# Kernel optimization log

Measured on AMD Instinct MI355X. Metric: run time of the kernel, lower is better.

The kernel has to match this reference:

```python
import jax, jax.numpy as jnp
import numpy as np

W_LOSS = 10.0
THRESHOLD = 1.0
ACOS_EPS = 1e-7


def _normalize(v, eps=1e-8):
    n = jnp.linalg.norm(v, axis=-1, keepdims=True)
    return v / jnp.maximum(n, eps)


def quat_to_rotmat(q):
    # q: (..., 4) in (w, x, y, z) order, as in Zhou et al. / EPN repo
    q = _normalize(q)
    w, x, y, z = q[..., 0], q[..., 1], q[..., 2], q[..., 3]
    R = jnp.stack([
        1 - 2 * (y * y + z * z), 2 * (x * y - z * w), 2 * (x * z + y * w),
        2 * (x * y + z * w), 1 - 2 * (x * x + z * z), 2 * (y * z - x * w),
        2 * (x * z - y * w), 2 * (y * z + x * w), 1 - 2 * (x * x + y * y),
    ], axis=-1)
    return R.reshape(q.shape[:-1] + (3, 3))


def acos_safe(x):
    return jnp.arccos(jnp.clip(x, -1.0 + ACOS_EPS, 1.0 - ACOS_EPS))


def angle_from_R(R):
    # R: (..., 3, 3) -> geodesic angle via trace
    tr = jnp.trace(R, axis1=-2, axis2=-1)
    return acos_safe(0.5 * (tr - 1.0))


def setup_inputs() -> dict:
    key = jax.random.key(0)
    k1, k2, k3, k4, k5 = jax.random.split(key, 5)
    B, NA, NR = 32768, 60, 4
    wts = jax.random.normal(k1, (B, NA), dtype=jnp.float32)
    label = jax.random.randint(k2, (B,), 0, NA, dtype=jnp.int64)
    y = jax.random.normal(k3, (B, NR, NA), dtype=jnp.float32)
    # gt_R and anchors are valid rotation matrices (via random quaternions)
    gt_R = quat_to_rotmat(jax.random.normal(k4, (B, NA, 4), dtype=jnp.float32))
    anchors = quat_to_rotmat(jax.random.normal(k5, (NA, 4), dtype=jnp.float32))
    return {"wts": wts, "label": label, "y": y, "gt_R": gt_R, "anchors": anchors}


def reference(wts, label, y, gt_R, anchors):
    b, na = wts.shape
    nr = y.shape[1]
    true_R = gt_R[:, 29]  # (b, 3, 3)

    # --- CrossEntropyLoss branch (classifier) ---
    logp = jax.nn.log_softmax(wts, axis=1)
    cls_loss = -jnp.mean(jnp.take_along_axis(logp, label[:, None], axis=1))
    preds = jnp.argmax(wts, axis=1)  # (b,)
    r_acc = jnp.mean((preds == label).astype(jnp.float32))

    # --- anchor-wise predicted rotations ---
    # y (b, nr, na) -> (b, na, nr) -> (b, na, 3, 3)
    pred_RAnchor = quat_to_rotmat(jnp.swapaxes(y, 1, 2))

    gt_bias = angle_from_R(gt_R)  # (b, na)
    mask = (gt_bias < THRESHOLD).astype(gt_R.dtype)[:, :, None, None]
    l2_loss = jnp.sum(jnp.square(gt_R * mask - pred_RAnchor * mask))
    loss = cls_loss + W_LOSS * l2_loss

    # --- final predicted rotation: gather best anchor, compose with anchor rot ---
    sel = jnp.take_along_axis(pred_RAnchor, preds[:, None, None, None], axis=1)[:, 0]  # (b,3,3)
    pred_R = jnp.einsum('bij,bjk->bik', anchors[preds], sel)

    # --- mean angular error ---
    ang_err = angle_from_R(jnp.einsum('bij,bkj->bik', pred_R, true_R))  # (b,)

    return (loss, cls_loss, W_LOSS * l2_loss, r_acc, ang_err)
```

## Files before the change

kernel.cpp:

```cpp
#include <hip/hip_runtime.h>
#include <math.h>

constexpr int Bc  = 32768;
constexpr int NAc = 60;

constexpr int BPB  = 4;
constexpr int NBLK = Bc / BPB;
constexpr int ROWF = NAc * 9;
constexpr int STG4 = BPB * ROWF / 4;

#define COS_ONE 0.5403023058681398f

__global__ __launch_bounds__(256) void mtl_all(
    const float* __restrict__ wts,
    const int*   __restrict__ label,
    const float* __restrict__ y,
    const float* __restrict__ gt_R,
    const float* __restrict__ anchors,
    float*       __restrict__ out,
    float*       __restrict__ l2p,
    float*       __restrict__ lpp,
    float*       __restrict__ crp)
{
    __shared__ __align__(16) float sg[BPB * ROWF + 16];
    const int tid  = threadIdx.x;
    const int lane = tid & 63;
    const int wave = tid >> 6;
    const int b0   = blockIdx.x * BPB;
    const int b    = b0 + wave;

    const float4* gb4 = (const float4*)(gt_R + (size_t)b0 * ROWF);
    float4* sg4 = (float4*)sg;
    sg4[tid]       = gb4[tid];
    sg4[tid + 256] = gb4[tid + 256];
    if (tid < STG4 - 512) sg4[tid + 512] = gb4[tid + 512];

    const int a = lane;
    int lab = label[b];
    float w = -INFINITY;
    float qw = 0, qx = 0, qy = 0, qz = 0;
    float A0=0,A1=0,A2=0,A3=0,A4=0,A5=0,A6=0,A7=0,A8=0;
    if (a < NAc) {
        w = wts[(size_t)b * NAc + a];
        const float* yb = y + (size_t)b * (4 * NAc) + a;
        qw = yb[0 * NAc];
        qx = yb[1 * NAc];
        qy = yb[2 * NAc];
        qz = yb[3 * NAc];
        const float* Ar = anchors + a * 9;
        A0 = Ar[0]; A1 = Ar[1]; A2 = Ar[2];
        A3 = Ar[3]; A4 = Ar[4]; A5 = Ar[5];
        A6 = Ar[6]; A7 = Ar[7]; A8 = Ar[8];
    }

    float n   = sqrtf(qw*qw + qx*qx + qy*qy + qz*qz);
    float inv = 1.0f / fmaxf(n, 1e-8f);
    float pw = qw*inv, px = qx*inv, py = qy*inv, pz = qz*inv;
    float R00 = 1.0f - 2.0f*(py*py + pz*pz);
    float R01 = 2.0f*(px*py - pz*pw);
    float R02 = 2.0f*(px*pz + py*pw);
    float R10 = 2.0f*(px*py + pz*pw);
    float R11 = 1.0f - 2.0f*(px*px + pz*pz);
    float R12 = 2.0f*(py*pz - px*pw);
    float R20 = 2.0f*(px*pz - py*pw);
    float R21 = 2.0f*(py*pz + px*pw);
    float R22 = 1.0f - 2.0f*(px*px + py*py);

    __syncthreads();

    float acc = 0.0f;
    if (a < NAc) {
        const float* g = sg + wave * ROWF + a * 9;
        float g0 = g[0], g1 = g[1], g2 = g[2];
        float g3 = g[3], g4 = g[4], g5 = g[5];
        float g6 = g[6], g7 = g[7], g8 = g[8];
        float xb = 0.5f * (g0 + g4 + g8 - 1.0f);
        if (xb > COS_ONE) {
            float d0 = g0-R00, d1 = g1-R01, d2 = g2-R02;
            float d3 = g3-R10, d4 = g4-R11, d5 = g5-R12;
            float d6 = g6-R20, d7 = g7-R21, d8 = g8-R22;
            acc = d0*d0 + d1*d1 + d2*d2
                + d3*d3 + d4*d4 + d5*d5
                + d6*d6 + d7*d7 + d8*d8;
        }
    }

    float mv = w;
    int   mi = lane;
    for (int off = 32; off; off >>= 1) {
        float ov = __shfl_xor(mv, off, 64);
        int   oi = __shfl_xor(mi, off, 64);
        if (ov > mv || (ov == mv && oi < mi)) { mv = ov; mi = oi; }
    }
    float e  = (a < NAc) ? expf(w - mv) : 0.0f;
    float se = e;
    for (int off = 32; off; off >>= 1) se += __shfl_xor(se, off, 64);
    float lse  = mv + logf(se);
    float wlab = __shfl(w, lab, 64);

    if (lane == mi) {
        float P00 = A0*R00 + A1*R10 + A2*R20;
        float P01 = A0*R01 + A1*R11 + A2*R21;
        float P02 = A0*R02 + A1*R12 + A2*R22;
        float P10 = A3*R00 + A4*R10 + A5*R20;
        float P11 = A3*R01 + A4*R11 + A5*R21;
        float P12 = A3*R02 + A4*R12 + A5*R22;
        float P20 = A6*R00 + A7*R10 + A8*R20;
        float P21 = A6*R01 + A7*R11 + A8*R21;
        float P22 = A6*R02 + A7*R12 + A8*R22;
        const float* tR = sg + wave * ROWF + 29 * 9;
        float tr = P00*tR[0] + P01*tR[1] + P02*tR[2]
                 + P10*tR[3] + P11*tR[4] + P12*tR[5]
                 + P20*tR[6] + P21*tR[7] + P22*tR[8];
        float cx = 0.5f * (tr - 1.0f);
        cx = fminf(fmaxf(cx, -1.0f + 1e-7f), 1.0f - 1e-7f);
        out[4 + b] = acosf(cx);
    }

    for (int off = 32; off; off >>= 1) acc += __shfl_xor(acc, off, 64);

    float* s_l2 = sg + BPB * ROWF;
    float* s_lp = s_l2 + 4;
    float* s_cr = s_lp + 4;
    if (lane == 0) {
        s_l2[wave] = acc;
        s_lp[wave] = wlab - lse;
        s_cr[wave] = (mi == lab) ? 1.0f : 0.0f;
    }
    __syncthreads();
    if (tid == 0) {
        l2p[blockIdx.x] = s_l2[0] + s_l2[1] + s_l2[2] + s_l2[3];
        lpp[blockIdx.x] = s_lp[0] + s_lp[1] + s_lp[2] + s_lp[3];
        crp[blockIdx.x] = s_cr[0] + s_cr[1] + s_cr[2] + s_cr[3];
    }
}

__global__ __launch_bounds__(256) void mtl_final(
    const float* __restrict__ l2p,
    const float* __restrict__ lpp,
    const float* __restrict__ crp,
    float*       __restrict__ out)
{
    const int tid  = threadIdx.x;
    const int lane = tid & 63;
    const int wave = tid >> 6;

    double l2 = 0.0, lp = 0.0, cr = 0.0;
    const float4* l2p4 = (const float4*)l2p;
    const float4* lpp4 = (const float4*)lpp;
    const float4* crp4 = (const float4*)crp;
    for (int i = tid; i < NBLK / 4; i += 256) {
        float4 v = l2p4[i];
        l2 += (double)v.x + (double)v.y + (double)v.z + (double)v.w;
        float4 u = lpp4[i];
        lp += (double)u.x + (double)u.y + (double)u.z + (double)u.w;
        float4 c = crp4[i];
        cr += (double)c.x + (double)c.y + (double)c.z + (double)c.w;
    }

    for (int off = 32; off; off >>= 1) {
        l2 += __shfl_xor(l2, off, 64);
        lp += __shfl_xor(lp, off, 64);
        cr += __shfl_xor(cr, off, 64);
    }
    __shared__ double s_l2[4], s_lp[4], s_cr[4];
    if (lane == 0) { s_l2[wave] = l2; s_lp[wave] = lp; s_cr[wave] = cr; }
    __syncthreads();
    if (tid == 0) {
        double t2 = s_l2[0] + s_l2[1] + s_l2[2] + s_l2[3];
        double tp = s_lp[0] + s_lp[1] + s_lp[2] + s_lp[3];
        double tc = s_cr[0] + s_cr[1] + s_cr[2] + s_cr[3];
        float cls = (float)(-tp / (double)Bc);
        float l2s = (float)(10.0 * t2);
        out[0] = cls + l2s;
        out[1] = cls;
        out[2] = l2s;
        out[3] = (float)(tc / (double)Bc);
    }
}

extern "C" void kernel_launch(void* const* d_in, const int* in_sizes, int n_in,
                              void* d_out, int out_size, void* d_ws, size_t ws_size,
                              hipStream_t stream) {
    const float* wts     = (const float*)d_in[0];
    const int*   label   = (const int*)d_in[1];
    const float* y       = (const float*)d_in[2];
    const float* gt_R    = (const float*)d_in[3];
    const float* anchors = (const float*)d_in[4];
    float* out = (float*)d_out;

    float* l2p = (float*)d_ws;
    float* lpp = l2p + NBLK;
    float* crp = lpp + NBLK;

    mtl_all  <<<NBLK, 256, 0, stream>>>(wts, label, y, gt_R, anchors,
                                        out, l2p, lpp, crp);
    mtl_final<<<1, 256, 0, stream>>>(l2p, lpp, crp, out);
}
```

Before: 140.1 us.

## Persistent grid with double-buffered async global-to-LDS staging of gt_R

The launch shrinks from one block per 4 batch rows to 2048 persistent blocks, each looping over 4 groups. The next group's gt_R tile is staged into a second LDS buffer with global_load_lds, and its wts, y and label are prefetched into registers while the current group is computed. The goal is to hide memory latency and overlap loads with compute, and also to cut the anchor loads and the partial-sum count. In exchange, occupancy and wave-level parallelism drop, and the code now depends on correct synchronisation around the async LDS loads.

```diff
diff --git a/kernel.cpp b/kernel.cpp
--- a/kernel.cpp
+++ b/kernel.cpp
@@ -1,15 +1,31 @@
 #include <hip/hip_runtime.h>
 #include <math.h>
 
-constexpr int Bc  = 32768;
-constexpr int NAc = 60;
+constexpr int Bc   = 32768;
+constexpr int NAc  = 60;
 
 constexpr int BPB  = 4;
-constexpr int NBLK = Bc / BPB;
+constexpr int PBLK = 2048;
+constexpr int ITER = Bc / (BPB * PBLK);
 constexpr int ROWF = NAc * 9;
-constexpr int STG4 = BPB * ROWF / 4;
+constexpr int GRPF = BPB * ROWF;
 
 #define COS_ONE 0.5403023058681398f
+
+typedef const __attribute__((address_space(1))) void* as1cv;
+typedef __attribute__((address_space(3)))       void* as3v;
+
+__device__ __forceinline__ void stage_group_async(const float* __restrict__ gt_R,
+                                                  int grp, float* lds,
+                                                  int wave, int lane)
+{
+    const float* gbase = gt_R + (size_t)grp * GRPF;
+    const int woff = wave * 512;
+    __builtin_amdgcn_global_load_lds((as1cv)(gbase + woff + lane * 4),
+                                     (as3v)(lds + woff), 16, 0, 0);
+    __builtin_amdgcn_global_load_lds((as1cv)(gbase + woff + 256 + lane * 4),
+                                     (as3v)(lds + woff + 256), 16, 0, 0);
+}
 
 __global__ __launch_bounds__(256) void mtl_all(
     const float* __restrict__ wts,
@@ -22,116 +38,144 @@
     float*       __restrict__ lpp,
     float*       __restrict__ crp)
 {
-    __shared__ __align__(16) float sg[BPB * ROWF + 16];
+    __shared__ __align__(16) float sg[2][GRPF];
+    __shared__ float s_red[12];
     const int tid  = threadIdx.x;
     const int lane = tid & 63;
     const int wave = tid >> 6;
-    const int b0   = blockIdx.x * BPB;
-    const int b    = b0 + wave;
-
-    const float4* gb4 = (const float4*)(gt_R + (size_t)b0 * ROWF);
-    float4* sg4 = (float4*)sg;
-    sg4[tid]       = gb4[tid];
-    sg4[tid + 256] = gb4[tid + 256];
-    if (tid < STG4 - 512) sg4[tid + 512] = gb4[tid + 512];
-
-    const int a = lane;
+    const int a    = lane;
+
+    float A0=0,A1=0,A2=0,A3=0,A4=0,A5=0,A6=0,A7=0,A8=0;
+    if (a < NAc) {
+        const float* Ar = anchors + a * 9;
+        A0=Ar[0]; A1=Ar[1]; A2=Ar[2];
+        A3=Ar[3]; A4=Ar[4]; A5=Ar[5];
+        A6=Ar[6]; A7=Ar[7]; A8=Ar[8];
+    }
+
+    int g = blockIdx.x;
+    {
+        stage_group_async(gt_R, g, sg[0], wave, lane);
+        const float4* gb4 = (const float4*)(gt_R + (size_t)g * GRPF);
+        if (tid < 28) ((float4*)sg[0])[512 + tid] = gb4[512 + tid];
+    }
+    int b   = g * BPB + wave;
     int lab = label[b];
-    float w = -INFINITY;
-    float qw = 0, qx = 0, qy = 0, qz = 0;
-    float A0=0,A1=0,A2=0,A3=0,A4=0,A5=0,A6=0,A7=0,A8=0;
+    float w = -INFINITY, qw=0, qx=0, qy=0, qz=0;
     if (a < NAc) {
         w = wts[(size_t)b * NAc + a];
         const float* yb = y + (size_t)b * (4 * NAc) + a;
-        qw = yb[0 * NAc];
-        qx = yb[1 * NAc];
-        qy = yb[2 * NAc];
-        qz = yb[3 * NAc];
-        const float* Ar = anchors + a * 9;
-        A0 = Ar[0]; A1 = Ar[1]; A2 = Ar[2];
-        A3 = Ar[3]; A4 = Ar[4]; A5 = Ar[5];
-        A6 = Ar[6]; A7 = Ar[7]; A8 = Ar[8];
-    }
-
-    float n   = sqrtf(qw*qw + qx*qx + qy*qy + qz*qz);
-    float inv = 1.0f / fmaxf(n, 1e-8f);
-    float pw = qw*inv, px = qx*inv, py = qy*inv, pz = qz*inv;
-    float R00 = 1.0f - 2.0f*(py*py + pz*pz);
-    float R01 = 2.0f*(px*py - pz*pw);
-    float R02 = 2.0f*(px*pz + py*pw);
-    float R10 = 2.0f*(px*py + pz*pw);
-    float R11 = 1.0f - 2.0f*(px*px + pz*pz);
-    float R12 = 2.0f*(py*pz - px*pw);
-    float R20 = 2.0f*(px*pz - py*pw);
-    float R21 = 2.0f*(py*pz + px*pw);
-    float R22 = 1.0f - 2.0f*(px*px + py*py);
-
+        qw = yb[0];  qx = yb[NAc];  qy = yb[2 * NAc];  qz = yb[3 * NAc];
+    }
     __syncthreads();
 
-    float acc = 0.0f;
-    if (a < NAc) {
-        const float* g = sg + wave * ROWF + a * 9;
-        float g0 = g[0], g1 = g[1], g2 = g[2];
-        float g3 = g[3], g4 = g[4], g5 = g[5];
-        float g6 = g[6], g7 = g[7], g8 = g[8];
-        float xb = 0.5f * (g0 + g4 + g8 - 1.0f);
-        if (xb > COS_ONE) {
-            float d0 = g0-R00, d1 = g1-R01, d2 = g2-R02;
-            float d3 = g3-R10, d4 = g4-R11, d5 = g5-R12;
-            float d6 = g6-R20, d7 = g7-R21, d8 = g8-R22;
-            acc = d0*d0 + d1*d1 + d2*d2
-                + d3*d3 + d4*d4 + d5*d5
-                + d6*d6 + d7*d7 + d8*d8;
-        }
-    }
-
-    float mv = w;
-    int   mi = lane;
-    for (int off = 32; off; off >>= 1) {
-        float ov = __shfl_xor(mv, off, 64);
-        int   oi = __shfl_xor(mi, off, 64);
-        if (ov > mv || (ov == mv && oi < mi)) { mv = ov; mi = oi; }
-    }
-    float e  = (a < NAc) ? expf(w - mv) : 0.0f;
-    float se = e;
-    for (int off = 32; off; off >>= 1) se += __shfl_xor(se, off, 64);
-    float lse  = mv + logf(se);
-    float wlab = __shfl(w, lab, 64);
-
-    if (lane == mi) {
-        float P00 = A0*R00 + A1*R10 + A2*R20;
-        float P01 = A0*R01 + A1*R11 + A2*R21;
-        float P02 = A0*R02 + A1*R12 + A2*R22;
-        float P10 = A3*R00 + A4*R10 + A5*R20;
-        float P11 = A3*R01 + A4*R11 + A5*R21;
-        float P12 = A3*R02 + A4*R12 + A5*R22;
-        float P20 = A6*R00 + A7*R10 + A8*R20;
-        float P21 = A6*R01 + A7*R11 + A8*R21;
-        float P22 = A6*R02 + A7*R12 + A8*R22;
-        const float* tR = sg + wave * ROWF + 29 * 9;
-        float tr = P00*tR[0] + P01*tR[1] + P02*tR[2]
-                 + P10*tR[3] + P11*tR[4] + P12*tR[5]
-                 + P20*tR[6] + P21*tR[7] + P22*tR[8];
-        float cx = 0.5f * (tr - 1.0f);
-        cx = fminf(fmaxf(cx, -1.0f + 1e-7f), 1.0f - 1e-7f);
-        out[4 + b] = acosf(cx);
-    }
-
-    for (int off = 32; off; off >>= 1) acc += __shfl_xor(acc, off, 64);
-
-    float* s_l2 = sg + BPB * ROWF;
-    float* s_lp = s_l2 + 4;
-    float* s_cr = s_lp + 4;
+    float l2acc = 0.0f, lpacc = 0.0f, cracc = 0.0f;
+
+    #pragma unroll
+    for (int it = 0; it < ITER; ++it) {
+        const int cur = it & 1, nxt = cur ^ 1;
+        const int gn  = g + PBLK;
+
+        float4 p2 = make_float4(0.f, 0.f, 0.f, 0.f);
+        int   labn = 0;
+        float wn = -INFINITY, qwn=0, qxn=0, qyn=0, qzn=0;
+        if (it + 1 < ITER) {
+            stage_group_async(gt_R, gn, sg[nxt], wave, lane);
+            const float4* nb4 = (const float4*)(gt_R + (size_t)gn * GRPF);
+            if (tid < 28) p2 = nb4[512 + tid];
+            const int bn = gn * BPB + wave;
+            labn = label[bn];
+            if (a < NAc) {
+                wn = wts[(size_t)bn * NAc + a];
+                const float* yb = y + (size_t)bn * (4 * NAc) + a;
+                qwn = yb[0];  qxn = yb[NAc];  qyn = yb[2 * NAc];  qzn = yb[3 * NAc];
+            }
+        }
+
+        float nq  = sqrtf(qw*qw + qx*qx + qy*qy + qz*qz);
+        float inv = 1.0f / fmaxf(nq, 1e-8f);
+        float pw = qw*inv, px = qx*inv, py = qy*inv, pz = qz*inv;
+        float R00 = 1.0f - 2.0f*(py*py + pz*pz);
+        float R01 = 2.0f*(px*py - pz*pw);
+        float R02 = 2.0f*(px*pz + py*pw);
+        float R10 = 2.0f*(px*py + pz*pw);
+        float R11 = 1.0f - 2.0f*(px*px + pz*pz);
+        float R12 = 2.0f*(py*pz - px*pw);
+        float R20 = 2.0f*(px*pz - py*pw);
+        float R21 = 2.0f*(py*pz + px*pw);
+        float R22 = 1.0f - 2.0f*(px*px + py*py);
+
+        if (a < NAc) {
+            const float* grow = sg[cur] + wave * ROWF + a * 9;
+            float g0 = grow[0], g1 = grow[1], g2 = grow[2];
+            float g3 = grow[3], g4 = grow[4], g5 = grow[5];
+            float g6 = grow[6], g7 = grow[7], g8 = grow[8];
+            float xb = 0.5f * (g0 + g4 + g8 - 1.0f);
+            if (xb > COS_ONE) {
+                float d0 = g0-R00, d1 = g1-R01, d2 = g2-R02;
+                float d3 = g3-R10, d4 = g4-R11, d5 = g5-R12;
+                float d6 = g6-R20, d7 = g7-R21, d8 = g8-R22;
+                l2acc += d0*d0 + d1*d1 + d2*d2
+                       + d3*d3 + d4*d4 + d5*d5
+                       + d6*d6 + d7*d7 + d8*d8;
+            }
+        }
+
+        float mv = w;
+        int   mi = lane;
+        for (int off = 32; off; off >>= 1) {
+            float ov = __shfl_xor(mv, off, 64);
+            int   oi = __shfl_xor(mi, off, 64);
+            if (ov > mv || (ov == mv && oi < mi)) { mv = ov; mi = oi; }
+        }
+        float e  = (a < NAc) ? expf(w - mv) : 0.0f;
+        float se = e;
+        for (int off = 32; off; off >>= 1) se += __shfl_xor(se, off, 64);
+        float lse  = mv + logf(se);
+        float wlab = __shfl(w, lab, 64);
+
+        lpacc += wlab - lse;
+        cracc += (mi == lab) ? 1.0f : 0.0f;
+
+        if (lane == mi) {
+            float P00 = A0*R00 + A1*R10 + A2*R20;
+            float P01 = A0*R01 + A1*R11 + A2*R21;
+            float P02 = A0*R02 + A1*R12 + A2*R22;
+            float P10 = A3*R00 + A4*R10 + A5*R20;
+            float P11 = A3*R01 + A4*R11 + A5*R21;
+            float P12 = A3*R02 + A4*R12 + A5*R22;
+            float P20 = A6*R00 + A7*R10 + A8*R20;
+            float P21 = A6*R01 + A7*R11 + A8*R21;
+            float P22 = A6*R02 + A7*R12 + A8*R22;
+            const float* tR = sg[cur] + wave * ROWF + 29 * 9;
+            float tr = P00*tR[0] + P01*tR[1] + P02*tR[2]
+                     + P10*tR[3] + P11*tR[4] + P12*tR[5]
+                     + P20*tR[6] + P21*tR[7] + P22*tR[8];
+            float cx = 0.5f * (tr - 1.0f);
+            cx = fminf(fmaxf(cx, -1.0f + 1e-7f), 1.0f - 1e-7f);
+            out[4 + b] = acosf(cx);
+        }
+
+        if (it + 1 < ITER) {
+            if (tid < 28) ((float4*)sg[nxt])[512 + tid] = p2;
+        }
+        __syncthreads();
+
+        w = wn; qw = qwn; qx = qxn; qy = qyn; qz = qzn;
+        lab = labn; g = gn; b = gn * BPB + wave;
+    }
+
+    for (int off = 32; off; off >>= 1) l2acc += __shfl_xor(l2acc, off, 64);
     if (lane == 0) {
-        s_l2[wave] = acc;
-        s_lp[wave] = wlab - lse;
-        s_cr[wave] = (mi == lab) ? 1.0f : 0.0f;
+        s_red[wave]     = l2acc;
+        s_red[4 + wave] = lpacc;
+        s_red[8 + wave] = cracc;
     }
     __syncthreads();
     if (tid == 0) {
-        l2p[blockIdx.x] = s_l2[0] + s_l2[1] + s_l2[2] + s_l2[3];
-        lpp[blockIdx.x] = s_lp[0] + s_lp[1] + s_lp[2] + s_lp[3];
-        crp[blockIdx.x] = s_cr[0] + s_cr[1] + s_cr[2] + s_cr[3];
+        l2p[blockIdx.x] = s_red[0] + s_red[1] + s_red[2]  + s_red[3];
+        lpp[blockIdx.x] = s_red[4] + s_red[5] + s_red[6]  + s_red[7];
+        crp[blockIdx.x] = s_red[8] + s_red[9] + s_red[10] + s_red[11];
     }
 }
 
@@ -149,7 +193,7 @@
     const float4* l2p4 = (const float4*)l2p;
     const float4* lpp4 = (const float4*)lpp;
     const float4* crp4 = (const float4*)crp;
-    for (int i = tid; i < NBLK / 4; i += 256) {
+    for (int i = tid; i < PBLK / 4; i += 256) {
         float4 v = l2p4[i];
         l2 += (double)v.x + (double)v.y + (double)v.z + (double)v.w;
         float4 u = lpp4[i];
@@ -190,10 +234,10 @@
     float* out = (float*)d_out;
 
     float* l2p = (float*)d_ws;
-    float* lpp = l2p + NBLK;
-    float* crp = lpp + NBLK;
-
-    mtl_all  <<<NBLK, 256, 0, stream>>>(wts, label, y, gt_R, anchors,
+    float* lpp = l2p + PBLK;
+    float* crp = lpp + PBLK;
+
+    mtl_all  <<<PBLK, 256, 0, stream>>>(wts, label, y, gt_R, anchors,
                                         out, l2p, lpp, crp);
     mtl_final<<<1, 256, 0, stream>>>(l2p, lpp, crp, out);
 }
```

Result: no change. 141.3 us (+0.9%).
